# Optimization experiments

Measured on AMD Instinct MI355X. Metric: run time of the kernel, lower is better.

Reference implementation:

```python
import jax, jax.numpy as jnp
import numpy as np

B, C, K = 8, 32, 512


def setup_inputs() -> dict:
    key = jax.random.key(0)
    k1, k2, k3 = jax.random.split(key, 3)
    amplitude = jax.random.normal(k1, (B, C, K), dtype=jnp.float32)
    phase = jax.random.normal(k2, (B, C, K), dtype=jnp.float32)
    A = jax.random.normal(k3, (K, K), dtype=jnp.float32)
    w_amplitude = jnp.float32(0.5)
    w_phase = jnp.float32(0.5)
    return {"amplitude": amplitude, "phase": phase, "A": A,
            "w_amplitude": w_amplitude, "w_phase": w_phase}


def reference(amplitude, phase, A, w_amplitude, w_phase):
    # amplitude, phase: (B, C, K)
    # pairwise differences along the frequency axis -> (B, C, K, K)
    amp_diff = amplitude[..., :, None] - amplitude[..., None, :]
    ph_diff = phase[..., :, None] - phase[..., None, :]
    fused = w_amplitude * amp_diff + w_phase * ph_diff
    # einsum('dd,bxcd->bxcd', A, fused): scale last axis by diag(A)
    temp = fused * jnp.diagonal(A)
    # einsum('bxcd,bxcd->bcd'): sum of squares over channel axis x=C -> (B, K, K)
    dist = jnp.sum(temp * temp, axis=1)
    exp_dist = 1.0 / (dist + 1e-10)
    eye = jnp.eye(K, dtype=exp_dist.dtype)
    offdiag = 1.0 - eye
    exp_dist = exp_dist * offdiag
    exp_max = jax.lax.stop_gradient(jnp.max(exp_dist, axis=-1, keepdims=True))
    p = exp_dist / exp_max
    p = (p * offdiag + eye) * 0.99  # probabilities in (0, 0.99]
    # bernoulli gumbel-softmax (hard, tau=1) with straight-through estimator
    logit = jnp.log(p / (1.0 - p))          # log(p/(1-p)); other class is -logit
    logits = jnp.stack([logit, -logit], axis=-1)  # (B, K, K, 2)
    gkey = jax.random.key(42)
    u = jax.random.uniform(gkey, logits.shape, minval=1e-10, maxval=1.0)
    gumbel = -jnp.log(-jnp.log(u))
    y_soft = jax.nn.softmax(logits + gumbel, axis=-1)
    idx = jnp.argmax(y_soft, axis=-1)
    y_hard = jax.nn.one_hot(idx, 2, dtype=y_soft.dtype)
    y = y_hard + y_soft - jax.lax.stop_gradient(y_soft)
    sample = y[..., 0]  # (B, K, K)
    return sample.mean(axis=0)  # (K, K)
```

## Files before the change

### kernel.cpp

```cpp
#include <hip/hip_runtime.h>
#include <stdint.h>
#include <math.h>

constexpr int NB = 8;
constexpr int NC = 32;
constexpr int NK = 512;
constexpr int ROWS = 4;

__device__ __forceinline__ uint32_t rotl32(uint32_t x, uint32_t r) {
    return (x << r) | (x >> (32u - r));
}

__device__ __forceinline__ uint32_t jax_random_bits(uint32_t n) {
    const uint32_t k0 = 0u, k1 = 42u;
    const uint32_t ks2 = k0 ^ k1 ^ 0x1BD11BDAu;
    uint32_t x0 = 0u + k0, x1 = n + k1;

    x0 += x1; x1 = rotl32(x1, 13); x1 ^= x0;
    x0 += x1; x1 = rotl32(x1, 15); x1 ^= x0;
    x0 += x1; x1 = rotl32(x1, 26); x1 ^= x0;
    x0 += x1; x1 = rotl32(x1,  6); x1 ^= x0;
    x0 += k1; x1 += ks2 + 1u;

    x0 += x1; x1 = rotl32(x1, 17); x1 ^= x0;
    x0 += x1; x1 = rotl32(x1, 29); x1 ^= x0;
    x0 += x1; x1 = rotl32(x1, 16); x1 ^= x0;
    x0 += x1; x1 = rotl32(x1, 24); x1 ^= x0;
    x0 += ks2; x1 += k0 + 2u;

    x0 += x1; x1 = rotl32(x1, 13); x1 ^= x0;
    x0 += x1; x1 = rotl32(x1, 15); x1 ^= x0;
    x0 += x1; x1 = rotl32(x1, 26); x1 ^= x0;
    x0 += x1; x1 = rotl32(x1,  6); x1 ^= x0;
    x0 += k0; x1 += k1 + 3u;

    x0 += x1; x1 = rotl32(x1, 17); x1 ^= x0;
    x0 += x1; x1 = rotl32(x1, 29); x1 ^= x0;
    x0 += x1; x1 = rotl32(x1, 16); x1 ^= x0;
    x0 += x1; x1 = rotl32(x1, 24); x1 ^= x0;
    x0 += k1; x1 += ks2 + 4u;

    x0 += x1; x1 = rotl32(x1, 13); x1 ^= x0;
    x0 += x1; x1 = rotl32(x1, 15); x1 ^= x0;
    x0 += x1; x1 = rotl32(x1, 26); x1 ^= x0;
    x0 += x1; x1 = rotl32(x1,  6); x1 ^= x0;
    x0 += ks2; x1 += k0 + 5u;

    return x0 ^ x1;
}

__device__ __forceinline__ float fastL(uint32_t bits, double& ud) {
    const double S = 1.0 - 1e-10, T = 1e-10;
    uint32_t fb = (bits >> 9) | 0x3F800000u;
    float bf = __uint_as_float(fb) - 1.0f;
    ud = (double)bf * S + T;
    if (bf <= 0.5f) {
        return -logf((float)ud);
    } else {
        double vm1 = S * ((double)bf - 1.0);
        return -log1pf((float)vm1);
    }
}

__device__ __noinline__ bool decide_slow(double a2, double c2,
                                         double u0, double u1) {
    return a2 * (-log(u1)) >= c2 * (-log(u0));
}

__global__ void prep_kernel(const float* __restrict__ amp,
                            const float* __restrict__ ph,
                            const float* __restrict__ A,
                            const float* __restrict__ wav,
                            const float* __restrict__ wpv,
                            double* __restrict__ F,
                            double* __restrict__ A2,
                            float* __restrict__ out) {
    int t = blockIdx.x * 256 + threadIdx.x;
    out[t] = 0.0f;
    if (t < NB * NC * NK) {
        double wa = (double)wav[0], wp = (double)wpv[0];
        F[t] = wa * (double)amp[t] + wp * (double)ph[t];
    }
    if (t < NK) {
        double a = (double)A[t * NK + t];
        A2[t] = a * a;
    }
}

__global__ __launch_bounds__(256) void sample_kernel(
    const double* __restrict__ F, const double* __restrict__ A2,
    float* __restrict__ out)
{
    const int i0   = blockIdx.x * ROWS;
    const int b    = blockIdx.y;
    const int tid  = threadIdx.x;
    const int j0   = 2 * tid;
    const int lane = tid & 63;
    const int wv   = tid >> 6;
    const int wjb  = wv * 128;

    __shared__ unsigned char wlist[4][ROWS][128];
    __shared__ double sred[ROWS][4];
    __shared__ double s_q[ROWS];

    const double* __restrict__ Fb = F + (size_t)b * NC * NK;

    double acc[2][ROWS];
    #pragma unroll
    for (int it = 0; it < 2; ++it)
        #pragma unroll
        for (int r = 0; r < ROWS; ++r) acc[it][r] = 0.0;

    #pragma unroll 8
    for (int c = 0; c < NC; ++c) {
        double fi_r[ROWS];
        #pragma unroll
        for (int r = 0; r < ROWS; ++r)
            fi_r[r] = Fb[c * NK + i0 + r];
        double2 fj = *(const double2*)(Fb + c * NK + j0);
        #pragma unroll
        for (int r = 0; r < ROWS; ++r) {
            double d0 = fi_r[r] - fj.x; acc[0][r] = fma(d0, d0, acc[0][r]);
            double d1 = fi_r[r] - fj.y; acc[1][r] = fma(d1, d1, acc[1][r]);
        }
    }

    double2 a2j = *(const double2*)(A2 + j0);
    double D[2][ROWS];
    #pragma unroll
    for (int r = 0; r < ROWS; ++r) {
        D[0][r] = acc[0][r] * a2j.x + 1e-10;
        D[1][r] = acc[1][r] * a2j.y + 1e-10;
    }

    #pragma unroll
    for (int r = 0; r < ROWS; ++r) {
        const int i = i0 + r;
        double m = 1e300;
        if (j0     != i) m = fmin(m, D[0][r]);
        if (j0 + 1 != i) m = fmin(m, D[1][r]);
        #pragma unroll
        for (int off = 32; off > 0; off >>= 1)
            m = fmin(m, __shfl_down(m, off));
        if (lane == 0) sred[r][wv] = m;
    }
    __syncthreads();
    if (tid < ROWS) {
        double m = fmin(fmin(sred[tid][0], sred[tid][1]),
                        fmin(sred[tid][2], sred[tid][3]));
        s_q[tid] = 0.99 * m;
    }
    __syncthreads();

    const unsigned long long ltmask = (1ull << lane) - 1ull;
    int nw[ROWS];
    #pragma unroll
    for (int r = 0; r < ROWS; ++r) {
        const int i = i0 + r;
        const double q = s_q[r];
        const double thr = 1.95e8 * (q * q);
        double t0 = D[0][r] - q;
        double t1 = D[1][r] - q;
        bool need0 = (j0     == i) || !(t0 * t0 > thr);
        bool need1 = (j0 + 1 == i) || !(t1 * t1 > thr);
        unsigned long long m0 = __ballot(need0);
        unsigned long long m1 = __ballot(need1);
        int c0 = __popcll(m0);
        nw[r] = c0 + __popcll(m1);
        if (need0) wlist[wv][r][__popcll(m0 & ltmask)]      = (unsigned char)(2 * lane);
        if (need1) wlist[wv][r][c0 + __popcll(m1 & ltmask)] = (unsigned char)(2 * lane + 1);
    }

    #pragma unroll
    for (int r = 0; r < ROWS; ++r) {
        const int i = i0 + r;
        const double q = s_q[r];
        const int n = nw[r];
        for (int k0v = 0; k0v < n; k0v += 64) {
            int k = k0v + lane;
            bool act = k < n;
            int jl = wlist[wv][r][act ? k : 0];
            int src = jl >> 1;
            double d0s = __shfl(D[0][r], src);
            double d1s = __shfl(D[1][r], src);
            double Dv = (jl & 1) ? d1s : d0s;
            int j = wjb + jl;

            double a2, c2;
            if (j == i) { a2 = 9801.0; c2 = 1.0; }
            else        { a2 = q * q; double t = Dv - q; c2 = t * t; }

            uint32_t n0 = 2u * (((uint32_t)(b * NK + i)) * NK + (uint32_t)j);
            bool hit = false;
            if (act) {
                uint32_t bits0 = jax_random_bits(n0);
                double u0d;
                float L0f = fastL(bits0, u0d);
                float L0lo = L0f * 0.99999f;
                if (!((double)c2 * (double)L0lo > 23.03 * a2)) {
                    uint32_t bits1 = jax_random_bits(n0 + 1u);
                    double u1d;
                    float L1f = fastL(bits1, u1d);
                    float lhs = (float)a2 * L1f;
                    float rhs = (float)c2 * L0f;
                    float diff = lhs - rhs;
                    if (fabsf(diff) > 1e-4f * (lhs + rhs))
                        hit = diff >= 0.0f;
                    else
                        hit = decide_slow(a2, c2, u0d, u1d);
                }
            }
            if (hit)
                atomicAdd(&out[i * NK + j], 0.125f);
        }
    }
}

extern "C" void kernel_launch(void* const* d_in, const int* in_sizes, int n_in,
                              void* d_out, int out_size, void* d_ws, size_t ws_size,
                              hipStream_t stream) {
    const float* amp = (const float*)d_in[0];
    const float* ph  = (const float*)d_in[1];
    const float* A   = (const float*)d_in[2];
    const float* wa  = (const float*)d_in[3];
    const float* wp  = (const float*)d_in[4];
    float* out = (float*)d_out;

    double* F  = (double*)d_ws;
    double* A2 = (double*)d_ws + NB * NC * NK;

    prep_kernel<<<1024, 256, 0, stream>>>(amp, ph, A, wa, wp, F, A2, out);

    dim3 grid(NK / ROWS, NB);
    sample_kernel<<<grid, 256, 0, stream>>>(F, A2, out);
}
```

Measured before the change: 85.12 us.

## Split sampling into filter and global compaction plus separate decide kernel

The fused per-block sampling loop is split in two. A filter kernel computes distances and appends candidate (row, j, D) entries to a global list via an atomic counter. A separate decide kernel then runs the RNG and decision over that compacted list in a grid-stride loop, so the expensive Threefry work is spread evenly instead of being serialized per wave. Rows per block drop from 4 to 2 for more blocks. The cost is an extra launch, global list traffic and an atomic per wave, and the list size depends on how many candidates survive the filter.

```diff
diff --git a/kernel.cpp b/kernel.cpp
--- a/kernel.cpp
+++ b/kernel.cpp
@@ -5,7 +5,9 @@
 constexpr int NB = 8;
 constexpr int NC = 32;
 constexpr int NK = 512;
-constexpr int ROWS = 4;
+constexpr int ROWS = 2;
+
+struct alignas(16) Entry { uint32_t tag; uint32_t pad; double D; };
 
 __device__ __forceinline__ uint32_t rotl32(uint32_t x, uint32_t r) {
     return (x << r) | (x >> (32u - r));
@@ -74,6 +76,7 @@
                             const float* __restrict__ wpv,
                             double* __restrict__ F,
                             double* __restrict__ A2,
+                            uint32_t* __restrict__ cnt,
                             float* __restrict__ out) {
     int t = blockIdx.x * 256 + threadIdx.x;
     out[t] = 0.0f;
@@ -85,11 +88,13 @@
         double a = (double)A[t * NK + t];
         A2[t] = a * a;
     }
-}
-
-__global__ __launch_bounds__(256) void sample_kernel(
+    if (t == 0) *cnt = 0;
+}
+
+__global__ __launch_bounds__(256) void filter_kernel(
     const double* __restrict__ F, const double* __restrict__ A2,
-    float* __restrict__ out)
+    double* __restrict__ qarr, uint32_t* __restrict__ cnt,
+    Entry* __restrict__ list)
 {
     const int i0   = blockIdx.x * ROWS;
     const int b    = blockIdx.y;
@@ -97,9 +102,7 @@
     const int j0   = 2 * tid;
     const int lane = tid & 63;
     const int wv   = tid >> 6;
-    const int wjb  = wv * 128;
-
-    __shared__ unsigned char wlist[4][ROWS][128];
+
     __shared__ double sred[ROWS][4];
     __shared__ double s_q[ROWS];
 
@@ -113,16 +116,13 @@
 
     #pragma unroll 8
     for (int c = 0; c < NC; ++c) {
-        double fi_r[ROWS];
-        #pragma unroll
-        for (int r = 0; r < ROWS; ++r)
-            fi_r[r] = Fb[c * NK + i0 + r];
+        double fr0 = Fb[c * NK + i0];
+        double fr1 = Fb[c * NK + i0 + 1];
         double2 fj = *(const double2*)(Fb + c * NK + j0);
-        #pragma unroll
-        for (int r = 0; r < ROWS; ++r) {
-            double d0 = fi_r[r] - fj.x; acc[0][r] = fma(d0, d0, acc[0][r]);
-            double d1 = fi_r[r] - fj.y; acc[1][r] = fma(d1, d1, acc[1][r]);
-        }
+        double d00 = fr0 - fj.x; acc[0][0] = fma(d00, d00, acc[0][0]);
+        double d10 = fr0 - fj.y; acc[1][0] = fma(d10, d10, acc[1][0]);
+        double d01 = fr1 - fj.x; acc[0][1] = fma(d01, d01, acc[0][1]);
+        double d11 = fr1 - fj.y; acc[1][1] = fma(d11, d11, acc[1][1]);
     }
 
     double2 a2j = *(const double2*)(A2 + j0);
@@ -148,12 +148,14 @@
     if (tid < ROWS) {
         double m = fmin(fmin(sred[tid][0], sred[tid][1]),
                         fmin(sred[tid][2], sred[tid][3]));
-        s_q[tid] = 0.99 * m;
+        double qv = 0.99 * m;
+        s_q[tid] = qv;
+        qarr[b * NK + i0 + tid] = qv;
     }
     __syncthreads();
 
     const unsigned long long ltmask = (1ull << lane) - 1ull;
-    int nw[ROWS];
+    bool need[2][ROWS];
     #pragma unroll
     for (int r = 0; r < ROWS; ++r) {
         const int i = i0 + r;
@@ -161,58 +163,80 @@
         const double thr = 1.95e8 * (q * q);
         double t0 = D[0][r] - q;
         double t1 = D[1][r] - q;
-        bool need0 = (j0     == i) || !(t0 * t0 > thr);
-        bool need1 = (j0 + 1 == i) || !(t1 * t1 > thr);
-        unsigned long long m0 = __ballot(need0);
-        unsigned long long m1 = __ballot(need1);
-        int c0 = __popcll(m0);
-        nw[r] = c0 + __popcll(m1);
-        if (need0) wlist[wv][r][__popcll(m0 & ltmask)]      = (unsigned char)(2 * lane);
-        if (need1) wlist[wv][r][c0 + __popcll(m1 & ltmask)] = (unsigned char)(2 * lane + 1);
-    }
-
-    #pragma unroll
-    for (int r = 0; r < ROWS; ++r) {
-        const int i = i0 + r;
-        const double q = s_q[r];
-        const int n = nw[r];
-        for (int k0v = 0; k0v < n; k0v += 64) {
-            int k = k0v + lane;
-            bool act = k < n;
-            int jl = wlist[wv][r][act ? k : 0];
-            int src = jl >> 1;
-            double d0s = __shfl(D[0][r], src);
-            double d1s = __shfl(D[1][r], src);
-            double Dv = (jl & 1) ? d1s : d0s;
-            int j = wjb + jl;
-
-            double a2, c2;
-            if (j == i) { a2 = 9801.0; c2 = 1.0; }
-            else        { a2 = q * q; double t = Dv - q; c2 = t * t; }
-
-            uint32_t n0 = 2u * (((uint32_t)(b * NK + i)) * NK + (uint32_t)j);
-            bool hit = false;
-            if (act) {
-                uint32_t bits0 = jax_random_bits(n0);
-                double u0d;
-                float L0f = fastL(bits0, u0d);
-                float L0lo = L0f * 0.99999f;
-                if (!((double)c2 * (double)L0lo > 23.03 * a2)) {
-                    uint32_t bits1 = jax_random_bits(n0 + 1u);
-                    double u1d;
-                    float L1f = fastL(bits1, u1d);
-                    float lhs = (float)a2 * L1f;
-                    float rhs = (float)c2 * L0f;
-                    float diff = lhs - rhs;
-                    if (fabsf(diff) > 1e-4f * (lhs + rhs))
-                        hit = diff >= 0.0f;
-                    else
-                        hit = decide_slow(a2, c2, u0d, u1d);
-                }
-            }
-            if (hit)
-                atomicAdd(&out[i * NK + j], 0.125f);
+        need[0][r] = (j0     == i) || !(t0 * t0 > thr);
+        need[1][r] = (j0 + 1 == i) || !(t1 * t1 > thr);
+    }
+    unsigned long long m00 = __ballot(need[0][0]);
+    unsigned long long m10 = __ballot(need[1][0]);
+    unsigned long long m01 = __ballot(need[0][1]);
+    unsigned long long m11 = __ballot(need[1][1]);
+    int c00 = __popcll(m00), c10 = __popcll(m10);
+    int c01 = __popcll(m01), c11 = __popcll(m11);
+    int total = c00 + c10 + c01 + c11;
+
+    int base = 0;
+    if (lane == 0) base = (int)atomicAdd(cnt, (uint32_t)total);
+    base = __shfl(base, 0);
+
+    const uint32_t rowtag0 = (uint32_t)(b * NK + i0) << 9;
+    const uint32_t rowtag1 = (uint32_t)(b * NK + i0 + 1) << 9;
+    if (need[0][0]) {
+        Entry e{rowtag0 | (uint32_t)j0, 0u, D[0][0]};
+        list[base + __popcll(m00 & ltmask)] = e;
+    }
+    if (need[1][0]) {
+        Entry e{rowtag0 | (uint32_t)(j0 + 1), 0u, D[1][0]};
+        list[base + c00 + __popcll(m10 & ltmask)] = e;
+    }
+    const int base2 = base + c00 + c10;
+    if (need[0][1]) {
+        Entry e{rowtag1 | (uint32_t)j0, 0u, D[0][1]};
+        list[base2 + __popcll(m01 & ltmask)] = e;
+    }
+    if (need[1][1]) {
+        Entry e{rowtag1 | (uint32_t)(j0 + 1), 0u, D[1][1]};
+        list[base2 + c01 + __popcll(m11 & ltmask)] = e;
+    }
+}
+
+__global__ __launch_bounds__(256) void decide_kernel(
+    const Entry* __restrict__ list, const uint32_t* __restrict__ cnt,
+    const double* __restrict__ qarr, float* __restrict__ out)
+{
+    const int n = (int)*cnt;
+    for (int k = blockIdx.x * 256 + threadIdx.x; k < n; k += gridDim.x * 256) {
+        Entry e = list[k];
+        const uint32_t tag = e.tag;
+        const int j   = (int)(tag & 511u);
+        const int row = (int)(tag >> 9);
+        const int i   = row & 511;
+        const double Dv = e.D;
+        const double q  = qarr[row];
+
+        double a2, c2;
+        if (j == i) { a2 = 9801.0; c2 = 1.0; }
+        else        { a2 = q * q; double t = Dv - q; c2 = t * t; }
+
+        const uint32_t n0 = 2u * ((uint32_t)row * (uint32_t)NK + (uint32_t)j);
+        bool hit = false;
+        uint32_t bits0 = jax_random_bits(n0);
+        double u0d;
+        float L0f = fastL(bits0, u0d);
+        float L0lo = L0f * 0.99999f;
+        if (!((double)c2 * (double)L0lo > 23.03 * a2)) {
+            uint32_t bits1 = jax_random_bits(n0 + 1u);
+            double u1d;
+            float L1f = fastL(bits1, u1d);
+            float lhs = (float)a2 * L1f;
+            float rhs = (float)c2 * L0f;
+            float diff = lhs - rhs;
+            if (fabsf(diff) > 1e-4f * (lhs + rhs))
+                hit = diff >= 0.0f;
+            else
+                hit = decide_slow(a2, c2, u0d, u1d);
         }
+        if (hit)
+            atomicAdd(&out[i * NK + j], 0.125f);
     }
 }
 
@@ -226,11 +250,17 @@
     const float* wp  = (const float*)d_in[4];
     float* out = (float*)d_out;
 
-    double* F  = (double*)d_ws;
-    double* A2 = (double*)d_ws + NB * NC * NK;
-
-    prep_kernel<<<1024, 256, 0, stream>>>(amp, ph, A, wa, wp, F, A2, out);
+    double*   F    = (double*)d_ws;
+    double*   A2   = F + NB * NC * NK;
+    double*   qarr = A2 + NK;
+    uint32_t* cnt  = (uint32_t*)(qarr + NB * NK);
+    Entry*    list = (Entry*)((char*)d_ws +
+                       ((size_t)(NB * NC * NK + NK + NB * NK) * 8 + 16));
+
+    prep_kernel<<<1024, 256, 0, stream>>>(amp, ph, A, wa, wp, F, A2, cnt, out);
 
     dim3 grid(NK / ROWS, NB);
-    sample_kernel<<<grid, 256, 0, stream>>>(F, A2, out);
-}
+    filter_kernel<<<grid, 256, 0, stream>>>(F, A2, qarr, cnt, list);
+
+    decide_kernel<<<2048, 256, 0, stream>>>(list, cnt, qarr, out);
+}
```

Result: slower. 167.8 us (+97.1%).
